# Performance work log

Hardware: AMD Instinct MI355X
Metric: run time of the kernel (lower is better)

The kernel has to match this reference:

```python
import jax, jax.numpy as jnp
import numpy as np

BIG = 1e8  # > max possible squared distance in a 64^3 volume (3*63^2 ~ 1.2e4)


def _edt(mask):
    """Exact Euclidean distance transform (scipy.ndimage.distance_transform_edt).

    mask: [B, X, Y, Z] float; distance at nonzero voxels to nearest zero voxel.
    Uses the exact separable squared-EDT: along each axis,
      g[i] = min_j f[j] + (i - j)^2  (lower envelope of parabolas, brute-forced).
    """
    f = jnp.where(mask > 0, BIG, 0.0).astype(jnp.float32)
    for ax in (1, 2, 3):
        f = jnp.moveaxis(f, ax, -1)            # [..., n]
        n = f.shape[-1]
        i = jnp.arange(n)
        d2 = ((i[:, None] - i[None, :]) ** 2).astype(jnp.float32)  # [n, n]
        f = jnp.min(f[..., None, :] + d2, axis=-1)                 # [..., n]
        f = jnp.moveaxis(f, -1, ax)
    return jnp.sqrt(f)


def _get_dist_map(mmap, label_inner, label_outer):
    lz = jnp.isin(mmap, jnp.asarray(label_outer)).astype(jnp.float32)
    lz = jnp.where(jnp.isin(mmap, jnp.asarray(label_inner)), 0.0, lz)
    tdm_outer = _edt(lz)                       # distance inside outer region to its zero set
    b = _edt(1.0 - lz)
    boundary = jnp.where(b == 1.0, 1.0, 0.0)   # boundary[boundary != 1] = 0
    outer = tdm_outer + boundary
    level_zero_inner = (outer == 0.0).astype(jnp.float32)
    tsd = -_edt(level_zero_inner) + tdm_outer  # signed distance
    return boundary, tsd


def setup_inputs() -> dict:
    key = jax.random.key(0)
    mmap = jax.random.randint(key, (2, 64, 64, 64), 0, 10, dtype=jnp.int32)
    return {"mmap": mmap}


def reference(mmap):
    d_mean = 2.0
    inner_boundary, phi_inner = _get_dist_map(mmap, [3, 5, 6, 7, 8, 9], [2, 1, 4, 0])
    outer_boundary, phi_outer = _get_dist_map(mmap, [3, 5, 6, 7, 8, 9, 2], [1, 4, 0])
    hausdorff_inner = jnp.abs(inner_boundary * phi_outer)
    hausdorff_outer = jnp.abs(outer_boundary * phi_inner)
    h_in_mean = hausdorff_inner.sum() / inner_boundary.sum()
    h_out_mean = hausdorff_outer.sum() / outer_boundary.sum()
    loss = (h_in_mean - d_mean) ** 2 + (h_out_mean - d_mean) ** 2
    return (h_in_mean, hausdorff_inner.max(), h_out_mean, hausdorff_outer.max(), loss)
```

## Files before the change

kernel.cpp:

```cpp
#include <hip/hip_runtime.h>
#include <hip/hip_bf16.h>
#include <math.h>

#define N 64
#define BATCH 2
#define PLANE (N * N)
#define VOL (BATCH * N * N * N)
#define BIGF 1e8f
#define LP 65
#define FBIG 3.4e38f
#define MASK1 0x17u
#define MASK2 0x13u


__global__ __launch_bounds__(512) void edt_yz(const int* __restrict__ mmap,
                                              float* __restrict__ ws) {
  __shared__ unsigned char colb[3][8][64];
  __shared__ unsigned long long colm[3][64];
  __shared__ unsigned long long zmT[64];
  __shared__ unsigned long long zmL[64];
  __shared__ float Bm1[N][LP];
  __shared__ float Bm2[N][LP];
  const int m = blockIdx.x >> 7;
  const int plane = blockIdx.x & 127;
  const int b = plane >> 6, x = plane & 63;
  const int t = threadIdx.x;
  const int z = t & 63, c = t >> 6;
  const unsigned lmask = m ? MASK2 : MASK1;
  const size_t bbase = (size_t)(b * N) * PLANE;

  #pragma unroll
  for (int p = 0; p < 3; ++p) {
    const int xp = x + p - 1;
    unsigned byte = 0;
    if (xp >= 0 && xp < N) {
      const size_t pb = bbase + (size_t)xp * PLANE;
      #pragma unroll
      for (int k = 0; k < 8; ++k) {
        const int y = 8 * c + k;
        byte |= ((lmask >> mmap[pb + y * N + z]) & 1u) << k;
      }
    }
    colb[p][c][z] = (unsigned char)byte;
  }
  __syncthreads();
  if (t < 192) {
    const int p = t >> 6, zz = t & 63;
    unsigned long long v = 0;
    #pragma unroll
    for (int cc = 0; cc < 8; ++cc)
      v |= (unsigned long long)colb[p][cc][zz] << (8 * cc);
    colm[p][zz] = v;
  }
  __syncthreads();
  if (t < 64) {
    const unsigned long long cx = colm[1][t];
    unsigned long long nb = colm[0][t] | colm[2][t] | (cx << 1) | (cx >> 1);
    if (t > 0) nb |= colm[1][t - 1];
    if (t < 63) nb |= colm[1][t + 1];
    zmT[t] = ~cx;
    zmL[t] = cx | nb;
    unsigned long long* bits =
        (unsigned long long*)(ws + (size_t)4 * VOL) + (size_t)m * (BATCH * N * N);
    bits[(size_t)(b * N + x) * N + t] = nb & ~cx;
  }
  __syncthreads();

  {
    const unsigned long long M0 = zmT[z];
    const unsigned long long M1 = zmL[z];
    const float zs = (float)(z * z);
    #pragma unroll
    for (int k = 0; k < 8; ++k) {
      const int y = 8 * c + k;
      {
        const unsigned long long lo = M0 << (63 - y);
        const int dl = __clzll((long long)lo);
        const int f = __ffsll((long long)(M0 >> y));
        const int d = min(dl, f ? (f - 1) : 99);
        Bm1[y][z] = (d > 63) ? BIGF : (float)(d * d) + zs;
      }
      {
        const unsigned long long lo = M1 << (63 - y);
        const int dl = __clzll((long long)lo);
        const int f = __ffsll((long long)(M1 >> y));
        const int d = min(dl, f ? (f - 1) : 99);
        Bm2[y][z] = (d > 63) ? BIGF : (float)(d * d) + zs;
      }
    }
  }
  __syncthreads();

  const int y = t & 63, w = t >> 6;
  float a1[8], a2[8], zq[8];
  #pragma unroll
  for (int q = 0; q < 8; ++q) { a1[q] = FBIG; a2[q] = FBIG; zq[q] = (float)(w + 8 * q); }
  float m2j = 0.f;
  #pragma unroll 2
  for (int j = 0; j < N; ++j) {
    const float f1 = Bm1[y][j];
    const float f2 = Bm2[y][j];
    #pragma unroll
    for (int q = 0; q < 8; ++q) {
      a1[q] = fminf(a1[q], fmaf(m2j, zq[q], f1));
      a2[q] = fminf(a2[q], fmaf(m2j, zq[q], f2));
    }
    m2j -= 2.f;
  }
  __syncthreads();
  #pragma unroll
  for (int q = 0; q < 8; ++q) {
    Bm1[y][w + 8 * q] = fmaf(zq[q], zq[q], a1[q]);
    Bm2[y][w + 8 * q] = fmaf(zq[q], zq[q], a2[q]);
  }
  __syncthreads();
  float* mid1 = ws + (size_t)m * VOL;
  float* mid2 = ws + (size_t)(2 + m) * VOL;
  const size_t pbase = (size_t)(b * N + x) * PLANE;
  #pragma unroll
  for (int k = 0; k < 8; ++k) {
    const int e = t + 512 * k;
    mid1[pbase + e] = Bm1[e >> 6][e & 63];
    mid2[pbase + e] = Bm2[e >> 6][e & 63];
  }
}

__global__ __launch_bounds__(256) void edt_x_fused(float* __restrict__ ws) {
  __shared__ float A1[N][LP];
  __shared__ float A2[N][LP];
  __shared__ float redS[4], redM[4], redB[4];
  const int m = blockIdx.x >> 7;
  const int plane = blockIdx.x & 127;
  const int b = plane >> 6, y = plane & 63;
  const int t = threadIdx.x;
  const int z = t & 63, w = t >> 6;

  const float* mid1 = ws + (size_t)m * VOL;
  const float* mid2 = ws + (size_t)(2 + m) * VOL;
  #pragma unroll
  for (int k = 0; k < 16; ++k) {
    const int e = t + 256 * k;
    const int xx = e >> 6, zz = e & 63;
    const float xs = (float)(xx * xx);
    const size_t idx = (size_t)(b * N + xx) * PLANE + y * N + zz;
    A1[xx][zz] = mid1[idx] + xs;
    A2[xx][zz] = mid2[idx] + xs;
  }
  __syncthreads();

  float a1[16], a2[16], xq[16];
  #pragma unroll
  for (int q = 0; q < 16; ++q) { a1[q] = FBIG; a2[q] = FBIG; xq[q] = (float)(w + 4 * q); }
  float m2j = 0.f;
  #pragma unroll 2
  for (int j = 0; j < N; ++j) {
    const float f1 = A1[j][z];
    const float f2 = A2[j][z];
    #pragma unroll
    for (int q = 0; q < 16; ++q) {
      a1[q] = fminf(a1[q], fmaf(m2j, xq[q], f1));
      a2[q] = fminf(a2[q], fmaf(m2j, xq[q], f2));
    }
    m2j -= 2.f;
  }

  const unsigned long long* bits =
      (const unsigned long long*)(ws + (size_t)4 * VOL) +
      (size_t)(m == 0 ? 1 : 0) * (BATCH * N * N);
  float hsum = 0.f, hmax = 0.f, bsum = 0.f;
  #pragma unroll
  for (int q = 0; q < 16; ++q) {
    const float e1 = fmaf(xq[q], xq[q], a1[q]);
    const float e2 = fmaf(xq[q], xq[q], a2[q]);
    const float tsd = sqrtf(e1) - sqrtf(e2);
    const int xx = w + 4 * q;
    const unsigned long long bv = bits[(size_t)(b * N + xx) * N + z];
    const float bnd = (float)((bv >> y) & 1ull);
    const float h = bnd * fabsf(tsd);
    hsum += h; bsum += bnd; hmax = fmaxf(hmax, h);
  }
  #pragma unroll
  for (int o = 32; o > 0; o >>= 1) {
    hsum += __shfl_down(hsum, o);
    bsum += __shfl_down(bsum, o);
    hmax = fmaxf(hmax, __shfl_down(hmax, o));
  }
  if (z == 0) { redS[w] = hsum; redB[w] = bsum; redM[w] = hmax; }
  __syncthreads();
  if (t == 0) {
    float* part = ws + (size_t)4 * VOL + 32768 + (size_t)blockIdx.x * 32;
    part[0] = redS[0] + redS[1] + redS[2] + redS[3];
    part[1] = redB[0] + redB[1] + redB[2] + redB[3];
    part[2] = fmaxf(fmaxf(redM[0], redM[1]), fmaxf(redM[2], redM[3]));
  }
}

__global__ __launch_bounds__(256) void final_k(const float* __restrict__ ws,
                                               float* __restrict__ out) {
  __shared__ float Ls[4], Lb[4], Lm[4];
  const int t = threadIdx.x;
  const float* part = ws + (size_t)4 * VOL + 32768;
  float s = part[(size_t)t * 32 + 0];
  float bsum = part[(size_t)t * 32 + 1];
  float mx = part[(size_t)t * 32 + 2];
  #pragma unroll
  for (int o = 32; o > 0; o >>= 1) {
    s += __shfl_down(s, o);
    bsum += __shfl_down(bsum, o);
    mx = fmaxf(mx, __shfl_down(mx, o));
  }
  const int wv = t >> 6;
  if ((t & 63) == 0) { Ls[wv] = s; Lb[wv] = bsum; Lm[wv] = mx; }
  __syncthreads();
  if (t == 0) {
    const float s_ho = Ls[0] + Ls[1], b2 = Lb[0] + Lb[1];
    const float mho = fmaxf(Lm[0], Lm[1]);
    const float s_hi = Ls[2] + Ls[3], b1 = Lb[2] + Lb[3];
    const float mhi = fmaxf(Lm[2], Lm[3]);
    const float him = s_hi / b1;
    const float hom = s_ho / b2;
    out[0] = him;
    out[1] = mhi;
    out[2] = hom;
    out[3] = mho;
    out[4] = (him - 2.f) * (him - 2.f) + (hom - 2.f) * (hom - 2.f);
  }
}

extern "C" void kernel_launch(void* const* d_in, const int* in_sizes, int n_in,
                              void* d_out, int out_size, void* d_ws,
                              size_t ws_size, hipStream_t stream) {
  (void)in_sizes; (void)n_in; (void)out_size; (void)ws_size;
  const int* mmap = (const int*)d_in[0];
  float* ws = (float*)d_ws;
  float* out = (float*)d_out;

  edt_yz<<<2 * BATCH * N, 512, 0, stream>>>(mmap, ws);
  edt_x_fused<<<2 * BATCH * N, 256, 0, stream>>>(ws);
  final_k<<<1, 256, 0, stream>>>(ws, out);
}
```

Measured before the change: 31.87 us.

## Store intermediate EDT as uint16, fuse final reduction via atomic counter, widen blocks

Intermediate squared distances are stored as 16-bit integers instead of floats, with 65535 as a sentinel for infinity, which halves the global memory traffic between the two EDT passes. The separate final reduction kernel is removed: each block of the x-pass publishes its partials, and the last block to finish, detected through an atomic counter, computes the outputs. The x-pass uses 512 threads with 8 outputs per thread instead of 256 threads with 16. In exchange the 16-bit store needs squared distances to stay below 65535, and the cross-block handoff depends on fences and on the counter being reset by the first kernel.

```diff
diff --git a/kernel.cpp b/kernel.cpp
--- a/kernel.cpp
+++ b/kernel.cpp
@@ -13,8 +13,12 @@
 #define MASK2 0x13u
 
 
+#define BITS_OFF ((size_t)8 * VOL)
+#define PART_OFF (BITS_OFF + (size_t)2 * BATCH * N * N * 8)
+#define CNT_OFF (PART_OFF + (size_t)256 * 8 * 4)
+
 __global__ __launch_bounds__(512) void edt_yz(const int* __restrict__ mmap,
-                                              float* __restrict__ ws) {
+                                              void* __restrict__ wsv) {
   __shared__ unsigned char colb[3][8][64];
   __shared__ unsigned long long colm[3][64];
   __shared__ unsigned long long zmT[64];
@@ -29,6 +33,8 @@
   const unsigned lmask = m ? MASK2 : MASK1;
   const size_t bbase = (size_t)(b * N) * PLANE;
 
+  if (blockIdx.x == 0 && t == 0) *(int*)((char*)wsv + CNT_OFF) = 0;
+
   #pragma unroll
   for (int p = 0; p < 3; ++p) {
     const int xp = x + p - 1;
@@ -61,7 +67,7 @@
     zmT[t] = ~cx;
     zmL[t] = cx | nb;
     unsigned long long* bits =
-        (unsigned long long*)(ws + (size_t)4 * VOL) + (size_t)m * (BATCH * N * N);
+        (unsigned long long*)((char*)wsv + BITS_OFF) + (size_t)m * (BATCH * N * N);
     bits[(size_t)(b * N + x) * N + t] = nb & ~cx;
   }
   __syncthreads();
@@ -114,50 +120,54 @@
     Bm2[y][w + 8 * q] = fmaf(zq[q], zq[q], a2[q]);
   }
   __syncthreads();
-  float* mid1 = ws + (size_t)m * VOL;
-  float* mid2 = ws + (size_t)(2 + m) * VOL;
+  unsigned short* mid1 = (unsigned short*)wsv + (size_t)m * VOL;
+  unsigned short* mid2 = (unsigned short*)wsv + (size_t)(2 + m) * VOL;
   const size_t pbase = (size_t)(b * N + x) * PLANE;
   #pragma unroll
   for (int k = 0; k < 8; ++k) {
     const int e = t + 512 * k;
-    mid1[pbase + e] = Bm1[e >> 6][e & 63];
-    mid2[pbase + e] = Bm2[e >> 6][e & 63];
+    mid1[pbase + e] = (unsigned short)fminf(Bm1[e >> 6][e & 63], 65535.f);
+    mid2[pbase + e] = (unsigned short)fminf(Bm2[e >> 6][e & 63], 65535.f);
   }
 }
 
-__global__ __launch_bounds__(256) void edt_x_fused(float* __restrict__ ws) {
+__global__ __launch_bounds__(512) void edt_x_fused(void* __restrict__ wsv,
+                                                   float* __restrict__ out) {
   __shared__ float A1[N][LP];
   __shared__ float A2[N][LP];
-  __shared__ float redS[4], redM[4], redB[4];
+  __shared__ float redS[8], redM[8], redB[8];
+  __shared__ int lastFlag;
   const int m = blockIdx.x >> 7;
   const int plane = blockIdx.x & 127;
   const int b = plane >> 6, y = plane & 63;
   const int t = threadIdx.x;
   const int z = t & 63, w = t >> 6;
 
-  const float* mid1 = ws + (size_t)m * VOL;
-  const float* mid2 = ws + (size_t)(2 + m) * VOL;
-  #pragma unroll
-  for (int k = 0; k < 16; ++k) {
-    const int e = t + 256 * k;
+  const unsigned short* mid1 = (const unsigned short*)wsv + (size_t)m * VOL;
+  const unsigned short* mid2 = (const unsigned short*)wsv + (size_t)(2 + m) * VOL;
+  #pragma unroll
+  for (int k = 0; k < 8; ++k) {
+    const int e = t + 512 * k;
     const int xx = e >> 6, zz = e & 63;
     const float xs = (float)(xx * xx);
     const size_t idx = (size_t)(b * N + xx) * PLANE + y * N + zz;
-    A1[xx][zz] = mid1[idx] + xs;
-    A2[xx][zz] = mid2[idx] + xs;
-  }
-  __syncthreads();
-
-  float a1[16], a2[16], xq[16];
-  #pragma unroll
-  for (int q = 0; q < 16; ++q) { a1[q] = FBIG; a2[q] = FBIG; xq[q] = (float)(w + 4 * q); }
+    const unsigned v1 = mid1[idx];
+    const unsigned v2 = mid2[idx];
+    A1[xx][zz] = ((v1 == 65535u) ? BIGF : (float)v1) + xs;
+    A2[xx][zz] = ((v2 == 65535u) ? BIGF : (float)v2) + xs;
+  }
+  __syncthreads();
+
+  float a1[8], a2[8], xq[8];
+  #pragma unroll
+  for (int q = 0; q < 8; ++q) { a1[q] = FBIG; a2[q] = FBIG; xq[q] = (float)(w + 8 * q); }
   float m2j = 0.f;
   #pragma unroll 2
   for (int j = 0; j < N; ++j) {
     const float f1 = A1[j][z];
     const float f2 = A2[j][z];
     #pragma unroll
-    for (int q = 0; q < 16; ++q) {
+    for (int q = 0; q < 8; ++q) {
       a1[q] = fminf(a1[q], fmaf(m2j, xq[q], f1));
       a2[q] = fminf(a2[q], fmaf(m2j, xq[q], f2));
     }
@@ -165,15 +175,15 @@
   }
 
   const unsigned long long* bits =
-      (const unsigned long long*)(ws + (size_t)4 * VOL) +
+      (const unsigned long long*)((char*)wsv + BITS_OFF) +
       (size_t)(m == 0 ? 1 : 0) * (BATCH * N * N);
   float hsum = 0.f, hmax = 0.f, bsum = 0.f;
   #pragma unroll
-  for (int q = 0; q < 16; ++q) {
+  for (int q = 0; q < 8; ++q) {
     const float e1 = fmaf(xq[q], xq[q], a1[q]);
     const float e2 = fmaf(xq[q], xq[q], a2[q]);
     const float tsd = sqrtf(e1) - sqrtf(e2);
-    const int xx = w + 4 * q;
+    const int xx = w + 8 * q;
     const unsigned long long bv = bits[(size_t)(b * N + xx) * N + z];
     const float bnd = (float)((bv >> y) & 1ull);
     const float h = bnd * fabsf(tsd);
@@ -187,43 +197,53 @@
   }
   if (z == 0) { redS[w] = hsum; redB[w] = bsum; redM[w] = hmax; }
   __syncthreads();
+
+  float* part = (float*)((char*)wsv + PART_OFF);
+  int* cnt = (int*)((char*)wsv + CNT_OFF);
   if (t == 0) {
-    float* part = ws + (size_t)4 * VOL + 32768 + (size_t)blockIdx.x * 32;
-    part[0] = redS[0] + redS[1] + redS[2] + redS[3];
-    part[1] = redB[0] + redB[1] + redB[2] + redB[3];
-    part[2] = fmaxf(fmaxf(redM[0], redM[1]), fmaxf(redM[2], redM[3]));
-  }
-}
-
-__global__ __launch_bounds__(256) void final_k(const float* __restrict__ ws,
-                                               float* __restrict__ out) {
-  __shared__ float Ls[4], Lb[4], Lm[4];
-  const int t = threadIdx.x;
-  const float* part = ws + (size_t)4 * VOL + 32768;
-  float s = part[(size_t)t * 32 + 0];
-  float bsum = part[(size_t)t * 32 + 1];
-  float mx = part[(size_t)t * 32 + 2];
-  #pragma unroll
-  for (int o = 32; o > 0; o >>= 1) {
-    s += __shfl_down(s, o);
-    bsum += __shfl_down(bsum, o);
-    mx = fmaxf(mx, __shfl_down(mx, o));
-  }
-  const int wv = t >> 6;
-  if ((t & 63) == 0) { Ls[wv] = s; Lb[wv] = bsum; Lm[wv] = mx; }
-  __syncthreads();
-  if (t == 0) {
-    const float s_ho = Ls[0] + Ls[1], b2 = Lb[0] + Lb[1];
-    const float mho = fmaxf(Lm[0], Lm[1]);
-    const float s_hi = Ls[2] + Ls[3], b1 = Lb[2] + Lb[3];
-    const float mhi = fmaxf(Lm[2], Lm[3]);
-    const float him = s_hi / b1;
-    const float hom = s_ho / b2;
-    out[0] = him;
-    out[1] = mhi;
-    out[2] = hom;
-    out[3] = mho;
-    out[4] = (him - 2.f) * (him - 2.f) + (hom - 2.f) * (hom - 2.f);
+    float s = 0.f, bs = 0.f, mx = 0.f;
+    #pragma unroll
+    for (int i = 0; i < 8; ++i) {
+      s += redS[i]; bs += redB[i]; mx = fmaxf(mx, redM[i]);
+    }
+    float* p = part + (size_t)blockIdx.x * 8;
+    p[0] = s; p[1] = bs; p[2] = mx;
+    __threadfence();
+    const int old = atomicAdd(cnt, 1);
+    lastFlag = (old == 255) ? 1 : 0;
+  }
+  __syncthreads();
+  if (lastFlag) {
+    __threadfence();
+    float s = 0.f, bs = 0.f, mx = 0.f;
+    if (t < 256) {
+      const float* p = part + (size_t)t * 8;
+      s = p[0]; bs = p[1]; mx = p[2];
+    }
+    #pragma unroll
+    for (int o = 32; o > 0; o >>= 1) {
+      s += __shfl_down(s, o);
+      bs += __shfl_down(bs, o);
+      mx = fmaxf(mx, __shfl_down(mx, o));
+    }
+    __syncthreads();
+    if ((t & 63) == 0 && t < 256) {
+      redS[t >> 6] = s; redB[t >> 6] = bs; redM[t >> 6] = mx;
+    }
+    __syncthreads();
+    if (t == 0) {
+      const float s_ho = redS[0] + redS[1], b2 = redB[0] + redB[1];
+      const float mho = fmaxf(redM[0], redM[1]);
+      const float s_hi = redS[2] + redS[3], b1 = redB[2] + redB[3];
+      const float mhi = fmaxf(redM[2], redM[3]);
+      const float him = s_hi / b1;
+      const float hom = s_ho / b2;
+      out[0] = him;
+      out[1] = mhi;
+      out[2] = hom;
+      out[3] = mho;
+      out[4] = (him - 2.f) * (him - 2.f) + (hom - 2.f) * (hom - 2.f);
+    }
   }
 }
 
@@ -232,10 +252,8 @@
                               size_t ws_size, hipStream_t stream) {
   (void)in_sizes; (void)n_in; (void)out_size; (void)ws_size;
   const int* mmap = (const int*)d_in[0];
-  float* ws = (float*)d_ws;
   float* out = (float*)d_out;
 
-  edt_yz<<<2 * BATCH * N, 512, 0, stream>>>(mmap, ws);
-  edt_x_fused<<<2 * BATCH * N, 256, 0, stream>>>(ws);
-  final_k<<<1, 256, 0, stream>>>(ws, out);
+  edt_yz<<<2 * BATCH * N, 512, 0, stream>>>(mmap, d_ws);
+  edt_x_fused<<<2 * BATCH * N, 512, 0, stream>>>(d_ws, out);
 }
```

New measurement: 31.74 us. No clear change (-0.4%).
